# Performance work log

Measured on AMD Instinct MI355X. Metric: run time of the kernel, lower is better.

Reference implementation:

```python
import jax, jax.numpy as jnp
import numpy as np


def _three_nn_interp(xyz1, xyz2, feat2):
    # squared Euclidean distances via gram trick, avoids (B,N,S,3) tensor
    # d2: (B, N, S)
    n1 = jnp.sum(xyz1 * xyz1, axis=-1)               # (B, N)
    n2 = jnp.sum(xyz2 * xyz2, axis=-1)               # (B, S)
    d2 = n1[:, :, None] + n2[:, None, :] - 2.0 * jnp.einsum('bnc,bsc->bns', xyz1, xyz2)
    d = jnp.sqrt(jnp.maximum(d2, 0.0))
    k = min(3, xyz2.shape[1])
    neg_d, idx = jax.lax.top_k(-d, k)                # smallest k distances
    dist = jnp.maximum(-neg_d, 1e-10)               # (B, N, k)
    w = 1.0 / dist
    w = w / jnp.sum(w, axis=-1, keepdims=True)
    # gather feat2 at idx: (B, N, k, C2)
    f2 = jnp.take_along_axis(feat2[:, None, :, :], idx[..., None], axis=2)
    return jnp.sum(f2 * w[..., None], axis=2)        # (B, N, C2)


def setup_inputs() -> dict:
    key = jax.random.key(0)
    ks = jax.random.split(key, 8)
    B, N, S, C1, C2, OUT = 8, 8192, 2048, 128, 256, 256
    IN = C1 + C2
    return {
        'xyz1': jax.random.normal(ks[0], (B, N, 3), dtype=jnp.float32),
        'xyz2': jax.random.normal(ks[1], (B, S, 3), dtype=jnp.float32),
        'feat1': jax.random.normal(ks[2], (B, N, C1), dtype=jnp.float32),
        'feat2': jax.random.normal(ks[3], (B, S, C2), dtype=jnp.float32),
        'W1': jax.random.normal(ks[4], (IN, OUT), dtype=jnp.float32) * (1.0 / np.sqrt(IN)),
        'b1': jnp.zeros((OUT,), dtype=jnp.float32),
        'W2': jax.random.normal(ks[5], (OUT, OUT), dtype=jnp.float32) * (1.0 / np.sqrt(OUT)),
        'b2': jnp.zeros((OUT,), dtype=jnp.float32),
    }


def reference(xyz1, xyz2, feat1, feat2, W1, b1, W2, b2):
    if xyz2.shape[1] == 1:
        interp = jnp.broadcast_to(feat2, (feat2.shape[0], xyz1.shape[1], feat2.shape[2]))
    else:
        interp = _three_nn_interp(xyz1, xyz2, feat2)
    x = jnp.concatenate([feat1, interp], axis=-1)    # (B, N, C1+C2)
    x = jax.nn.relu(x @ W1 + b1)
    x = jax.nn.relu(x @ W2 + b2)
    return x
```

## Files before the change

### kernel.cpp

```cpp
#include <hip/hip_runtime.h>
#include <hip/hip_bf16.h>

#define BB   8
#define NN   8192
#define SS   2048
#define C1C  128
#define C2C  256
#define KIN  384
#define OUTC 256

typedef __attribute__((ext_vector_type(4))) float f32x4;
typedef __attribute__((ext_vector_type(8))) short short8;
typedef __attribute__((ext_vector_type(8))) unsigned short ushortx8;

__device__ __forceinline__ ushort f2bf(float v) {
    __hip_bfloat16 h = __float2bfloat16(v);
    return __builtin_bit_cast(ushort, h);
}

__device__ __forceinline__ float med3(float a, float b, float c) {
    return __builtin_amdgcn_fmed3f(a, b, c);
}

__global__ __launch_bounds__(1024, 8) void knn_gather_prep_kernel(
    const float* __restrict__ xyz1, const float* __restrict__ xyz2,
    const float* __restrict__ feat2, ushort* __restrict__ interpB,
    const float* __restrict__ W1, ushort* __restrict__ W1pack,
    const float* __restrict__ W2, ushort* __restrict__ W2pack)
{
    __shared__ float4 sp[SS];
    __shared__ int   sIdx[128][3];
    __shared__ float sW[128][3];

    const int tid   = threadIdx.x;
    const int b     = blockIdx.x & 7;
    const int chunk = blockIdx.x >> 3;
    const int qbase = chunk << 7;

    const float* x2 = xyz2 + (size_t)b * SS * 3;
    for (int i = tid; i < SS; i += 1024) {
        float x = x2[i*3+0], y = x2[i*3+1], z = x2[i*3+2];
        sp[i] = make_float4(-2.f*x, -2.f*y, -2.f*z, x*x + y*y + z*z);
    }

    {
        const int idx = blockIdx.x * 1024 + tid;
        const int n1 = 12 * 16 * 512;
        if (idx < n1) {
            int o = idx;
            int e = o & 7, lane = (o >> 3) & 63, j = (o >> 9) & 3;
            int wc = (o >> 11) & 3, s = o >> 13;
            int n = wc * 64 + j * 16 + (lane & 15);
            int k = s * 32 + (lane >> 4) * 8 + e;
            W1pack[o] = f2bf(W1[(size_t)k * OUTC + n]);
        } else if (idx < n1 + OUTC * OUTC) {
            int o = idx - n1;
            int e = o & 7, lane = (o >> 3) & 63, j = (o >> 9) & 3;
            int wc = (o >> 11) & 3, s = o >> 13;
            int n = wc * 64 + j * 16 + (lane & 15);
            int k = s * 32 + (lane >> 4) * 8 + e;
            W2pack[o] = f2bf(W2[(size_t)k * OUTC + n]);
        }
    }
    __syncthreads();

    const int g = tid >> 4;
    const int l = tid & 15;
    const int qa = qbase + g * 2;

    const float* qp = xyz1 + ((size_t)b * NN + qa) * 3;
    float px[2] = {qp[0], qp[3]};
    float py[2] = {qp[1], qp[4]};
    float pz[2] = {qp[2], qp[5]};

    float c0[2], c1[2], c2[2];
#pragma unroll
    for (int qi = 0; qi < 2; ++qi) { c0[qi] = c1[qi] = c2[qi] = 1e30f; }

    for (int jj = 0; jj < 128; jj += 4) {
        float4 P[4];
#pragma unroll
        for (int u = 0; u < 4; ++u) P[u] = sp[((jj + u) << 4) + l];
#pragma unroll
        for (int u = 0; u < 4; ++u) {
#pragma unroll
            for (int qi = 0; qi < 2; ++qi) {
                float f = fmaf(px[qi], P[u].x,
                          fmaf(py[qi], P[u].y,
                          fmaf(pz[qi], P[u].z, P[u].w)));
                c2[qi] = med3(f, c1[qi], c2[qi]);
                c1[qi] = med3(f, c0[qi], c1[qi]);
                c0[qi] = fminf(f, c0[qi]);
            }
        }
    }

#pragma unroll
    for (int m = 1; m <= 8; m <<= 1) {
#pragma unroll
        for (int qi = 0; qi < 2; ++qi) {
            float b0 = __shfl_xor(c0[qi], m);
            float b1 = __shfl_xor(c1[qi], m);
            float b2 = __shfl_xor(c2[qi], m);
            float bv[3] = {b0, b1, b2};
#pragma unroll
            for (int e = 0; e < 3; ++e) {
                float d = bv[e];
                c2[qi] = med3(d, c1[qi], c2[qi]);
                c1[qi] = med3(d, c0[qi], c1[qi]);
                c0[qi] = fminf(d, c0[qi]);
            }
        }
    }
    const float t0 = c2[0], t1 = c2[1];

    float e0[2], e1[2], e2[2];
    int   i0[2], i1[2], i2[2];
#pragma unroll
    for (int qi = 0; qi < 2; ++qi) {
        e0[qi] = e1[qi] = e2[qi] = 1e30f;
        i0[qi] = i1[qi] = i2[qi] = 0x3fffffff;
    }

    for (int jj = 0; jj < 128; jj += 4) {
        float4 P[4];
#pragma unroll
        for (int u = 0; u < 4; ++u) P[u] = sp[((jj + u) << 4) + l];
#pragma unroll
        for (int u = 0; u < 4; ++u) {
            const int s = ((jj + u) << 4) + l;
#pragma unroll
            for (int qi = 0; qi < 2; ++qi) {
                float f = fmaf(px[qi], P[u].x,
                          fmaf(py[qi], P[u].y,
                          fmaf(pz[qi], P[u].z, P[u].w)));
                float tq = qi ? t1 : t0;
                if (f <= tq) {
                    bool lt2 = (f < e2[qi]) || (f == e2[qi] && s < i2[qi]);
                    if (lt2) {
                        bool lt1 = (f < e1[qi]) || (f == e1[qi] && s < i1[qi]);
                        bool lt0 = (f < e0[qi]) || (f == e0[qi] && s < i0[qi]);
                        e2[qi] = lt1 ? e1[qi] : f;  i2[qi] = lt1 ? i1[qi] : s;
                        e1[qi] = lt0 ? e0[qi] : (lt1 ? f : e1[qi]);
                        i1[qi] = lt0 ? i0[qi] : (lt1 ? s : i1[qi]);
                        e0[qi] = lt0 ? f : e0[qi];  i0[qi] = lt0 ? s : i0[qi];
                    }
                }
            }
        }
    }

#pragma unroll
    for (int m = 1; m <= 8; m <<= 1) {
#pragma unroll
        for (int qi = 0; qi < 2; ++qi) {
            float ob0 = __shfl_xor(e0[qi], m), ob1 = __shfl_xor(e1[qi], m), ob2 = __shfl_xor(e2[qi], m);
            int   oj0 = __shfl_xor(i0[qi], m), oj1 = __shfl_xor(i1[qi], m), oj2 = __shfl_xor(i2[qi], m);
            float dv[3] = {ob0, ob1, ob2}; int iv[3] = {oj0, oj1, oj2};
#pragma unroll
            for (int e = 0; e < 3; ++e) {
                float d = dv[e]; int s = iv[e];
                bool lt2 = (d < e2[qi]) || (d == e2[qi] && s < i2[qi]);
                if (lt2) {
                    bool lt1 = (d < e1[qi]) || (d == e1[qi] && s < i1[qi]);
                    bool lt0 = (d < e0[qi]) || (d == e0[qi] && s < i0[qi]);
                    e2[qi] = lt1 ? e1[qi] : d;  i2[qi] = lt1 ? i1[qi] : s;
                    e1[qi] = lt0 ? e0[qi] : (lt1 ? d : e1[qi]);
                    i1[qi] = lt0 ? i0[qi] : (lt1 ? s : i1[qi]);
                    e0[qi] = lt0 ? d : e0[qi];  i0[qi] = lt0 ? s : i0[qi];
                }
            }
        }
    }

    if (l == 0) {
#pragma unroll
        for (int qi = 0; qi < 2; ++qi) {
            float nx = px[qi], ny = py[qi], nz = pz[qi];
            float n1 = nx*nx + ny*ny + nz*nz;
            float d0 = sqrtf(fmaxf(n1 + e0[qi], 0.f));
            float d1 = sqrtf(fmaxf(n1 + e1[qi], 0.f));
            float d2s = sqrtf(fmaxf(n1 + e2[qi], 0.f));
            float w0 = 1.f / fmaxf(d0, 1e-10f);
            float w1 = 1.f / fmaxf(d1, 1e-10f);
            float w2 = 1.f / fmaxf(d2s, 1e-10f);
            float wsum = w0 + w1 + w2;
            int qq = g * 2 + qi;
            sIdx[qq][0] = i0[qi]; sIdx[qq][1] = i1[qi]; sIdx[qq][2] = i2[qi];
            sW[qq][0] = w0 / wsum; sW[qq][1] = w1 / wsum; sW[qq][2] = w2 / wsum;
        }
    }
    __syncthreads();

    const int wid = tid >> 6, lane = tid & 63;
    for (int qq = wid; qq < 128; qq += 16) {
        int a0 = sIdx[qq][0], a1 = sIdx[qq][1], a2 = sIdx[qq][2];
        float w0 = sW[qq][0], w1 = sW[qq][1], w2 = sW[qq][2];
        const float4* r0 = (const float4*)(feat2 + ((size_t)b * SS + a0) * C2C);
        const float4* r1 = (const float4*)(feat2 + ((size_t)b * SS + a1) * C2C);
        const float4* r2 = (const float4*)(feat2 + ((size_t)b * SS + a2) * C2C);
        float4 v0 = r0[lane], v1 = r1[lane], v2 = r2[lane];
        ushort4 o;
        o.x = f2bf(w0*v0.x + w1*v1.x + w2*v2.x);
        o.y = f2bf(w0*v0.y + w1*v1.y + w2*v2.y);
        o.z = f2bf(w0*v0.z + w1*v1.z + w2*v2.z);
        o.w = f2bf(w0*v0.w + w1*v1.w + w2*v2.w);
        *(ushort4*)(interpB + ((size_t)b * NN + qbase + qq) * C2C + lane * 4) = o;
    }
}

#define GBM 128
#define GBN 256
#define GBK 32

__device__ __forceinline__ void gld_lds16(const void* g, void* l) {
    __builtin_amdgcn_global_load_lds(
        (const __attribute__((address_space(1))) void*)g,
        (__attribute__((address_space(3))) void*)l, 16, 0, 0);
}

__global__ __launch_bounds__(512, 4) void gemm_fused(
    const float* __restrict__ feat1,
    const ushort* __restrict__ interpB,
    const ushort* __restrict__ W1pack, const float* __restrict__ b1,
    const ushort* __restrict__ W2pack, const float* __restrict__ b2,
    float* __restrict__ out)
{
    __shared__ ushort pool[GBM * 256];

    const int tid  = threadIdx.x;
    const int lane = tid & 63;
    const int wid  = tid >> 6;
    const int m0   = blockIdx.x * GBM;
    const int wr   = wid >> 2;
    const int wc   = wid & 3;

    const int rsub = lane >> 2;
    const int slot = lane & 3;
    const int csub = slot * 8;
    const int usw  = (slot ^ (rsub & 3)) * 8;

    const int kgrp = (lane >> 4) * 8;
    const int rl   = lane & 15;
    const int ksw  = kgrp ^ ((rl & 3) << 3);
    const int cl   = lane & 15;
    const int rgrp = (lane >> 4) * 4;

    auto stageA = [&](int k0, int buf) {
        ushort* sAb = pool + buf * 4096;
        const int r = m0 + wid * 16 + rsub;
        if (k0 < C1C) {
            const float* src = feat1 + (size_t)r * C1C + k0 + usw;
            float4 u = ((const float4*)src)[0];
            float4 v = ((const float4*)src)[1];
            ushortx8 t;
            t[0] = f2bf(u.x); t[1] = f2bf(u.y); t[2] = f2bf(u.z); t[3] = f2bf(u.w);
            t[4] = f2bf(v.x); t[5] = f2bf(v.y); t[6] = f2bf(v.z); t[7] = f2bf(v.w);
            *(ushortx8*)&sAb[wid * 512 + rsub * 32 + csub] = t;
        } else {
            gld_lds16(interpB + (size_t)r * C2C + (k0 - C1C) + usw, &sAb[wid * 512]);
        }
    };

    f32x4 acc1[4][4];
#pragma unroll
    for (int i = 0; i < 4; ++i)
#pragma unroll
        for (int j = 0; j < 4; ++j) acc1[i][j] = (f32x4){0.f, 0.f, 0.f, 0.f};

    int cur = 0;
    stageA(0, 0);
    short8 bfc[4], bfn[4];
#pragma unroll
    for (int j = 0; j < 4; ++j)
        bfc[j] = *(const short8*)&W1pack[(size_t)(0 * 16 + wc * 4 + j) * 512 + lane * 8];

    for (int k0 = 0, s = 0; k0 < KIN; k0 += GBK, ++s) {
        __syncthreads();
        if (k0 + GBK < KIN) {
            stageA(k0 + GBK, cur ^ 1);
#pragma unroll
            for (int j = 0; j < 4; ++j)
                bfn[j] = *(const short8*)&W1pack[(size_t)((s + 1) * 16 + wc * 4 + j) * 512 + lane * 8];
        }

        const ushort* sAb = pool + cur * 4096;
        short8 af[4];
#pragma unroll
        for (int i = 0; i < 4; ++i)
            af[i] = *(const short8*)&sAb[(wr * 64 + i * 16 + rl) * GBK + ksw];
#pragma unroll
        for (int i = 0; i < 4; ++i)
#pragma unroll
            for (int j = 0; j < 4; ++j)
                acc1[i][j] = __builtin_amdgcn_mfma_f32_16x16x32_bf16(
                    af[i], bfc[j], acc1[i][j], 0, 0, 0);
#pragma unroll
        for (int j = 0; j < 4; ++j) bfc[j] = bfn[j];
        cur ^= 1;
    }
    __syncthreads();

#pragma unroll
    for (int j = 0; j < 4; ++j)
        bfc[j] = *(const short8*)&W2pack[(size_t)(0 * 16 + wc * 4 + j) * 512 + lane * 8];

#pragma unroll
    for (int j = 0; j < 4; ++j) {
        const int c = wc * 64 + j * 16 + cl;
        const float bv = b1[c];
        const int u = c >> 3, sub = c & 7;
#pragma unroll
        for (int i = 0; i < 4; ++i) {
#pragma unroll
            for (int rr = 0; rr < 4; ++rr) {
                const int r = wr * 64 + i * 16 + rgrp + rr;
                const float v = fmaxf(acc1[i][j][rr] + bv, 0.f);
                pool[r * 256 + ((u ^ (r & 31)) << 3) + sub] = f2bf(v);
            }
        }
    }
    __syncthreads();

    f32x4 acc2[4][4];
#pragma unroll
    for (int i = 0; i < 4; ++i)
#pragma unroll
        for (int j = 0; j < 4; ++j) acc2[i][j] = (f32x4){0.f, 0.f, 0.f, 0.f};

    for (int s = 0; s < 8; ++s) {
        if (s < 7) {
#pragma unroll
            for (int j = 0; j < 4; ++j)
                bfn[j] = *(const short8*)&W2pack[(size_t)((s + 1) * 16 + wc * 4 + j) * 512 + lane * 8];
        }
        const int ub = s * 4 + (lane >> 4);
        short8 af[4];
#pragma unroll
        for (int i = 0; i < 4; ++i) {
            const int r = wr * 64 + i * 16 + rl;
            af[i] = *(const short8*)&pool[r * 256 + ((ub ^ (r & 31)) << 3)];
        }
#pragma unroll
        for (int i = 0; i < 4; ++i)
#pragma unroll
            for (int j = 0; j < 4; ++j)
                acc2[i][j] = __builtin_amdgcn_mfma_f32_16x16x32_bf16(
                    af[i], bfc[j], acc2[i][j], 0, 0, 0);
#pragma unroll
        for (int j = 0; j < 4; ++j) bfc[j] = bfn[j];
    }

#pragma unroll
    for (int j = 0; j < 4; ++j) {
        const int col = wc * 64 + j * 16 + cl;
        const float bv = b2[col];
#pragma unroll
        for (int i = 0; i < 4; ++i) {
            const int rowb = m0 + wr * 64 + i * 16 + rgrp;
#pragma unroll
            for (int rr = 0; rr < 4; ++rr) {
                out[(size_t)(rowb + rr) * OUTC + col] =
                    fmaxf(acc2[i][j][rr] + bv, 0.f);
            }
        }
    }
}

extern "C" void kernel_launch(void* const* d_in, const int* in_sizes, int n_in,
                              void* d_out, int out_size, void* d_ws, size_t ws_size,
                              hipStream_t stream) {
    const float* xyz1  = (const float*)d_in[0];
    const float* xyz2  = (const float*)d_in[1];
    const float* feat1 = (const float*)d_in[2];
    const float* feat2 = (const float*)d_in[3];
    const float* W1    = (const float*)d_in[4];
    const float* b1    = (const float*)d_in[5];
    const float* W2    = (const float*)d_in[6];
    const float* b2    = (const float*)d_in[7];
    float* out = (float*)d_out;

    char* ws = (char*)d_ws;
    ushort* interpB = (ushort*)(ws);
    ushort* W1pack  = (ushort*)(ws + 33554432);
    ushort* W2pack  = (ushort*)(ws + 33751040);

    const int M = BB * NN;

    knn_gather_prep_kernel<<<512, 1024, 0, stream>>>(xyz1, xyz2, feat2, interpB,
                                                     W1, W1pack, W2, W2pack);

    gemm_fused<<<M / GBM, 512, 0, stream>>>(feat1, interpB,
                                            W1pack, b1, W2pack, b2, out);
}
```

Measured before the change: 97.54 us.

## Prune 3-NN search with x-coordinate bucketing of reference points

```diff
diff --git a/kernel.cpp b/kernel.cpp
--- a/kernel.cpp
+++ b/kernel.cpp
@@ -22,6 +22,11 @@
     return __builtin_amdgcn_fmed3f(a, b, c);
 }
 
+__device__ __forceinline__ int xbucket(float x) {
+    int b = (int)floorf((x + 4.0f) * 32.0f);
+    return min(max(b, 0), 255);
+}
+
 __global__ __launch_bounds__(1024, 8) void knn_gather_prep_kernel(
     const float* __restrict__ xyz1, const float* __restrict__ xyz2,
     const float* __restrict__ feat2, ushort* __restrict__ interpB,
@@ -29,18 +34,25 @@
     const float* __restrict__ W2, ushort* __restrict__ W2pack)
 {
     __shared__ float4 sp[SS];
-    __shared__ int   sIdx[128][3];
-    __shared__ float sW[128][3];
+    __shared__ int    ssid[SS];
+    __shared__ int    cnt[256];
+    __shared__ int    cnt2[256];
+    __shared__ int    sIdx[128][3];
+    __shared__ float  sW[128][3];
 
     const int tid   = threadIdx.x;
     const int b     = blockIdx.x & 7;
     const int chunk = blockIdx.x >> 3;
     const int qbase = chunk << 7;
 
+    if (tid < 256) { cnt[tid] = 0; cnt2[tid] = 0; }
+    __syncthreads();
+
     const float* x2 = xyz2 + (size_t)b * SS * 3;
     for (int i = tid; i < SS; i += 1024) {
         float x = x2[i*3+0], y = x2[i*3+1], z = x2[i*3+2];
         sp[i] = make_float4(-2.f*x, -2.f*y, -2.f*z, x*x + y*y + z*z);
+        atomicAdd(&cnt[xbucket(x)], 1);
     }
 
     {
@@ -64,130 +76,128 @@
     }
     __syncthreads();
 
+    for (int d = 1; d < 256; d <<= 1) {
+        int v = 0;
+        if (tid < 256) {
+            v = cnt[tid];
+            if (tid >= d) v += cnt[tid - d];
+        }
+        __syncthreads();
+        if (tid < 256) cnt[tid] = v;
+        __syncthreads();
+    }
+
+    for (int i = tid; i < SS; i += 1024) {
+        float x = -0.5f * sp[i].x;
+        int bq = xbucket(x);
+        int base = (bq == 0) ? 0 : cnt[bq - 1];
+        int pos = base + atomicAdd(&cnt2[bq], 1);
+        ssid[pos] = i;
+    }
+    __syncthreads();
+
     const int g = tid >> 4;
     const int l = tid & 15;
     const int qa = qbase + g * 2;
 
     const float* qp = xyz1 + ((size_t)b * NN + qa) * 3;
-    float px[2] = {qp[0], qp[3]};
-    float py[2] = {qp[1], qp[4]};
-    float pz[2] = {qp[2], qp[5]};
-
-    float c0[2], c1[2], c2[2];
-#pragma unroll
-    for (int qi = 0; qi < 2; ++qi) { c0[qi] = c1[qi] = c2[qi] = 1e30f; }
-
-    for (int jj = 0; jj < 128; jj += 4) {
-        float4 P[4];
-#pragma unroll
-        for (int u = 0; u < 4; ++u) P[u] = sp[((jj + u) << 4) + l];
-#pragma unroll
-        for (int u = 0; u < 4; ++u) {
-#pragma unroll
-            for (int qi = 0; qi < 2; ++qi) {
-                float f = fmaf(px[qi], P[u].x,
-                          fmaf(py[qi], P[u].y,
-                          fmaf(pz[qi], P[u].z, P[u].w)));
-                c2[qi] = med3(f, c1[qi], c2[qi]);
-                c1[qi] = med3(f, c0[qi], c1[qi]);
-                c0[qi] = fminf(f, c0[qi]);
-            }
-        }
-    }
-
-#pragma unroll
-    for (int m = 1; m <= 8; m <<= 1) {
-#pragma unroll
-        for (int qi = 0; qi < 2; ++qi) {
-            float b0 = __shfl_xor(c0[qi], m);
-            float b1 = __shfl_xor(c1[qi], m);
-            float b2 = __shfl_xor(c2[qi], m);
+    float pxa[2] = {qp[0], qp[3]};
+    float pya[2] = {qp[1], qp[4]};
+    float pza[2] = {qp[2], qp[5]};
+
+#pragma unroll
+    for (int qi = 0; qi < 2; ++qi) {
+        const float px = pxa[qi], py = pya[qi], pz = pza[qi];
+        const float n1 = px*px + py*py + pz*pz;
+
+        int cb = xbucket(px);
+        int c  = (cb == 0) ? 0 : cnt[cb - 1];
+        int w0 = min(max(c - 128, 0), SS - 256);
+        float a0 = 1e30f, a1 = 1e30f, a2 = 1e30f;
+#pragma unroll
+        for (int u = 0; u < 16; ++u) {
+            int o = ssid[w0 + u * 16 + l];
+            float4 P = sp[o];
+            float f = fmaf(px, P.x, fmaf(py, P.y, fmaf(pz, P.z, P.w)));
+            a2 = med3(f, a1, a2);
+            a1 = med3(f, a0, a1);
+            a0 = fminf(f, a0);
+        }
+#pragma unroll
+        for (int m = 1; m <= 8; m <<= 1) {
+            float b0 = __shfl_xor(a0, m);
+            float b1 = __shfl_xor(a1, m);
+            float b2 = __shfl_xor(a2, m);
             float bv[3] = {b0, b1, b2};
 #pragma unroll
             for (int e = 0; e < 3; ++e) {
                 float d = bv[e];
-                c2[qi] = med3(d, c1[qi], c2[qi]);
-                c1[qi] = med3(d, c0[qi], c1[qi]);
-                c0[qi] = fminf(d, c0[qi]);
+                a2 = med3(d, a1, a2);
+                a1 = med3(d, a0, a1);
+                a0 = fminf(d, a0);
             }
         }
-    }
-    const float t0 = c2[0], t1 = c2[1];
-
-    float e0[2], e1[2], e2[2];
-    int   i0[2], i1[2], i2[2];
-#pragma unroll
-    for (int qi = 0; qi < 2; ++qi) {
-        e0[qi] = e1[qi] = e2[qi] = 1e30f;
-        i0[qi] = i1[qi] = i2[qi] = 0x3fffffff;
-    }
-
-    for (int jj = 0; jj < 128; jj += 4) {
-        float4 P[4];
-#pragma unroll
-        for (int u = 0; u < 4; ++u) P[u] = sp[((jj + u) << 4) + l];
-#pragma unroll
-        for (int u = 0; u < 4; ++u) {
-            const int s = ((jj + u) << 4) + l;
-#pragma unroll
-            for (int qi = 0; qi < 2; ++qi) {
-                float f = fmaf(px[qi], P[u].x,
-                          fmaf(py[qi], P[u].y,
-                          fmaf(pz[qi], P[u].z, P[u].w)));
-                float tq = qi ? t1 : t0;
-                if (f <= tq) {
-                    bool lt2 = (f < e2[qi]) || (f == e2[qi] && s < i2[qi]);
-                    if (lt2) {
-                        bool lt1 = (f < e1[qi]) || (f == e1[qi] && s < i1[qi]);
-                        bool lt0 = (f < e0[qi]) || (f == e0[qi] && s < i0[qi]);
-                        e2[qi] = lt1 ? e1[qi] : f;  i2[qi] = lt1 ? i1[qi] : s;
-                        e1[qi] = lt0 ? e0[qi] : (lt1 ? f : e1[qi]);
-                        i1[qi] = lt0 ? i0[qi] : (lt1 ? s : i1[qi]);
-                        e0[qi] = lt0 ? f : e0[qi];  i0[qi] = lt0 ? s : i0[qi];
-                    }
-                }
+
+        float r2 = fmaxf(a2 + n1, 0.f);
+        float rx = sqrtf(r2) * 1.001f;
+        int blo = xbucket(px - rx);
+        int bhi = xbucket(px + rx);
+        int lo2 = (blo == 0) ? 0 : cnt[blo - 1];
+        int ub  = cnt[bhi];
+
+        float e0 = 1e30f, e1 = 1e30f, e2 = 1e30f;
+        int   i0 = 0x3fffffff, i1 = 0x3fffffff, i2 = 0x3fffffff;
+        for (int s0 = lo2; s0 < ub; s0 += 16) {
+            int slot = s0 + l;
+            if (slot < ub) {
+                int o = ssid[slot];
+                float4 P = sp[o];
+                float f = fmaf(px, P.x, fmaf(py, P.y, fmaf(pz, P.z, P.w)));
+                bool lt2 = (f < e2) || (f == e2 && o < i2);
+                bool lt1 = (f < e1) || (f == e1 && o < i1);
+                bool lt0 = (f < e0) || (f == e0 && o < i0);
+                float ne2 = lt1 ? e1 : (lt2 ? f : e2);
+                int   ni2 = lt1 ? i1 : (lt2 ? o : i2);
+                float ne1 = lt0 ? e0 : (lt1 ? f : e1);
+                int   ni1 = lt0 ? i0 : (lt1 ? o : i1);
+                float ne0 = lt0 ? f : e0;
+                int   ni0 = lt0 ? o : i0;
+                e2 = ne2; i2 = ni2; e1 = ne1; i1 = ni1; e0 = ne0; i0 = ni0;
             }
         }
-    }
-
-#pragma unroll
-    for (int m = 1; m <= 8; m <<= 1) {
-#pragma unroll
-        for (int qi = 0; qi < 2; ++qi) {
-            float ob0 = __shfl_xor(e0[qi], m), ob1 = __shfl_xor(e1[qi], m), ob2 = __shfl_xor(e2[qi], m);
-            int   oj0 = __shfl_xor(i0[qi], m), oj1 = __shfl_xor(i1[qi], m), oj2 = __shfl_xor(i2[qi], m);
+
+#pragma unroll
+        for (int m = 1; m <= 8; m <<= 1) {
+            float ob0 = __shfl_xor(e0, m), ob1 = __shfl_xor(e1, m), ob2 = __shfl_xor(e2, m);
+            int   oj0 = __shfl_xor(i0, m), oj1 = __shfl_xor(i1, m), oj2 = __shfl_xor(i2, m);
             float dv[3] = {ob0, ob1, ob2}; int iv[3] = {oj0, oj1, oj2};
 #pragma unroll
             for (int e = 0; e < 3; ++e) {
                 float d = dv[e]; int s = iv[e];
-                bool lt2 = (d < e2[qi]) || (d == e2[qi] && s < i2[qi]);
-                if (lt2) {
-                    bool lt1 = (d < e1[qi]) || (d == e1[qi] && s < i1[qi]);
-                    bool lt0 = (d < e0[qi]) || (d == e0[qi] && s < i0[qi]);
-                    e2[qi] = lt1 ? e1[qi] : d;  i2[qi] = lt1 ? i1[qi] : s;
-                    e1[qi] = lt0 ? e0[qi] : (lt1 ? d : e1[qi]);
-                    i1[qi] = lt0 ? i0[qi] : (lt1 ? s : i1[qi]);
-                    e0[qi] = lt0 ? d : e0[qi];  i0[qi] = lt0 ? s : i0[qi];
-                }
+                bool lt2 = (d < e2) || (d == e2 && s < i2);
+                bool lt1 = (d < e1) || (d == e1 && s < i1);
+                bool lt0 = (d < e0) || (d == e0 && s < i0);
+                float ne2 = lt1 ? e1 : (lt2 ? d : e2);
+                int   ni2 = lt1 ? i1 : (lt2 ? s : i2);
+                float ne1 = lt0 ? e0 : (lt1 ? d : e1);
+                int   ni1 = lt0 ? i0 : (lt1 ? s : i1);
+                float ne0 = lt0 ? d : e0;
+                int   ni0 = lt0 ? s : i0;
+                e2 = ne2; i2 = ni2; e1 = ne1; i1 = ni1; e0 = ne0; i0 = ni0;
             }
         }
-    }
-
-    if (l == 0) {
-#pragma unroll
-        for (int qi = 0; qi < 2; ++qi) {
-            float nx = px[qi], ny = py[qi], nz = pz[qi];
-            float n1 = nx*nx + ny*ny + nz*nz;
-            float d0 = sqrtf(fmaxf(n1 + e0[qi], 0.f));
-            float d1 = sqrtf(fmaxf(n1 + e1[qi], 0.f));
-            float d2s = sqrtf(fmaxf(n1 + e2[qi], 0.f));
-            float w0 = 1.f / fmaxf(d0, 1e-10f);
-            float w1 = 1.f / fmaxf(d1, 1e-10f);
-            float w2 = 1.f / fmaxf(d2s, 1e-10f);
-            float wsum = w0 + w1 + w2;
+
+        if (l == 0) {
+            float d0 = sqrtf(fmaxf(n1 + e0, 0.f));
+            float d1 = sqrtf(fmaxf(n1 + e1, 0.f));
+            float d2s = sqrtf(fmaxf(n1 + e2, 0.f));
+            float w0v = 1.f / fmaxf(d0, 1e-10f);
+            float w1v = 1.f / fmaxf(d1, 1e-10f);
+            float w2v = 1.f / fmaxf(d2s, 1e-10f);
+            float wsum = w0v + w1v + w2v;
             int qq = g * 2 + qi;
-            sIdx[qq][0] = i0[qi]; sIdx[qq][1] = i1[qi]; sIdx[qq][2] = i2[qi];
-            sW[qq][0] = w0 / wsum; sW[qq][1] = w1 / wsum; sW[qq][2] = w2 / wsum;
+            sIdx[qq][0] = i0; sIdx[qq][1] = i1; sIdx[qq][2] = i2;
+            sW[qq][0] = w0v / wsum; sW[qq][1] = w1v / wsum; sW[qq][2] = w2v / wsum;
         }
     }
     __syncthreads();
```

After: 124.4 us. 27.5% more time.
